# Optimization experiments

Hardware: AMD Instinct MI355X
Metric: run time of the kernel (lower is better)

The kernel has to match this reference:

```python
import jax, jax.numpy as jnp
import numpy as np

B, L, D = 8, 2048, 1024
PAD = 512  # trailing padded positions (zeros) to exercise the two padding masks


def setup_inputs() -> dict:
    key = jax.random.key(0)
    ks = jax.random.split(key, 11)
    q = jax.random.normal(ks[0], (B, L, D), dtype=jnp.float32)
    k = jax.random.normal(ks[1], (B, L, D), dtype=jnp.float32)
    v = jax.random.normal(ks[2], (B, L, D), dtype=jnp.float32)
    # zero-pad trailing positions (module infers masks from zero rows)
    q = q.at[:, L - PAD:, :].set(0.0)
    k = k.at[:, L - PAD:, :].set(0.0)
    v = v.at[:, L - PAD:, :].set(0.0)
    s = 1.0 / np.sqrt(D)
    Wq = jax.random.normal(ks[3], (D, D), dtype=jnp.float32) * s
    bq = jax.random.normal(ks[4], (D,), dtype=jnp.float32) * 0.01
    Wk = jax.random.normal(ks[5], (D, D), dtype=jnp.float32) * s
    bk = jax.random.normal(ks[6], (D,), dtype=jnp.float32) * 0.01
    Wv = jax.random.normal(ks[7], (D, D), dtype=jnp.float32) * s
    bv = jax.random.normal(ks[8], (D,), dtype=jnp.float32) * 0.01
    Wo = jax.random.normal(ks[9], (D, D), dtype=jnp.float32) * s
    bo = jax.random.normal(ks[10], (D,), dtype=jnp.float32) * 0.01
    return {"q": q, "k": k, "v": v, "Wq": Wq, "bq": bq, "Wk": Wk, "bk": bk,
            "Wv": Wv, "bv": bv, "Wo": Wo, "bo": bo}


def reference(q, k, v, Wq, bq, Wk, bk, Wv, bv, Wo, bo):
    # masks computed from raw (pre-projection) q, k, exactly like padding_mask_k/_q
    # bmm(ones_like(q), k^T)[b,i,j] == sum_d k[b,j,d]  -> mask where k row sums to 0
    attn_mask = (jnp.sum(k, axis=-1) == 0.0)[:, None, :]      # [B,1,Lk] -> broadcast [B,Lq,Lk]
    softmax_mask = (jnp.sum(q, axis=-1) == 0.0)[:, :, None]    # [B,Lq,1]

    qp = q @ Wq.T + bq  # torch Linear: x W^T + b
    kp = k @ Wk.T + bk
    vp = v @ Wv.T + bv

    scale = vp.shape[-1] ** -0.5  # original overwrites passed `scale`
    att = jnp.einsum('bqd,bkd->bqk', qp, kp) * scale           # [B,Lq,Lk]
    att = jnp.where(attn_mask, -jnp.inf, att)
    att = jax.nn.softmax(att, axis=-1)
    att = jnp.where(softmax_mask, 0.0, att)

    out = jnp.einsum('bqk,bkd->bqd', att, vp)                  # [B,Lq,D]
    out = out @ Wo.T + bo
    x = out + qp  # residual uses the PROJECTED q
    # LayerNorm, elementwise_affine=False, eps=1e-5
    mu = jnp.mean(x, axis=-1, keepdims=True)
    var = jnp.mean(jnp.square(x - mu), axis=-1, keepdims=True)
    return (x - mu) / jnp.sqrt(var + 1e-5)
```

## Files before the change

kernel.cpp:

```cpp
#include <hip/hip_runtime.h>
#include <stdint.h>

typedef unsigned short u16;
typedef __attribute__((ext_vector_type(8))) short short8;
typedef __attribute__((ext_vector_type(4))) float f32x4;

#define B_ 8
#define L_ 2048
#define D_ 1024

__device__ __forceinline__ u16 f2bf(float f) {
    unsigned int u = __float_as_uint(f);
    u = u + 0x7FFFu + ((u >> 16) & 1u);
    return (u16)(u >> 16);
}
__device__ __forceinline__ float bf2f(u16 h) {
    return __uint_as_float(((unsigned int)h) << 16);
}

struct CM3 {
    const float* s[3];
    u16* d[3];
    int* m[3];
};
__global__ __launch_bounds__(256) void convmask3_kernel(CM3 c) {
    int sel = blockIdx.y;
    const float* x = c.s[sel];
    u16* xb = c.d[sel];
    int* mask = c.m[sel];
    long row = blockIdx.x;
    int t = threadIdx.x;
    float4 v = ((const float4*)(x + row * D_))[t];
    ushort4 o;
    o.x = f2bf(v.x); o.y = f2bf(v.y); o.z = f2bf(v.z); o.w = f2bf(v.w);
    ((ushort4*)(xb + row * D_))[t] = o;
    float s = v.x + v.y + v.z + v.w;
    #pragma unroll
    for (int off = 32; off; off >>= 1) s += __shfl_down(s, off);
    __shared__ float sh[4];
    if ((t & 63) == 0) sh[t >> 6] = s;
    __syncthreads();
    if (t == 0) {
        float tot = sh[0] + sh[1] + sh[2] + sh[3];
        mask[row] = (tot == 0.0f) ? 1 : 0;
    }
}

struct Ptr4 { const float* s0; const float* s1; const float* s2; const float* s3; };
__global__ __launch_bounds__(256) void convert4_kernel(Ptr4 p, u16* __restrict__ dst) {
    const float* srcs[4] = {p.s0, p.s1, p.s2, p.s3};
    const float* src = srcs[blockIdx.y];
    u16* d = dst + (size_t)blockIdx.y * D_ * D_;
    int i = blockIdx.x * 256 + threadIdx.x;
    float4 v = ((const float4*)src)[i];
    ushort4 o;
    o.x = f2bf(v.x); o.y = f2bf(v.y); o.z = f2bf(v.z); o.w = f2bf(v.w);
    ((ushort4*)d)[i] = o;
}

__global__ __launch_bounds__(256) void flags_kernel(const int* __restrict__ mq,
                                                    const int* __restrict__ mk,
                                                    const int* __restrict__ mv,
                                                    int* __restrict__ q128,
                                                    int* __restrict__ k128,
                                                    int* __restrict__ v128,
                                                    int* __restrict__ k32) {
    int b = blockIdx.x, t = threadIdx.x;
    const int* src; int* dst; int g; int n;
    if (b < 128)      { src = mq; dst = q128; g = b;       n = 128; }
    else if (b < 256) { src = mk; dst = k128; g = b - 128; n = 128; }
    else if (b < 384) { src = mv; dst = v128; g = b - 256; n = 128; }
    else              { src = mk; dst = k32;  g = b - 384; n = 32;  }
    int val = (t < n) ? src[(long)g * n + t] : 1;
    __shared__ int sh;
    if (t == 0) sh = 1;
    __syncthreads();
    if (!val) sh = 0;
    __syncthreads();
    if (t == 0) dst[g] = sh;
}

__global__ __launch_bounds__(512) void packbits_kernel(const int* __restrict__ k32,
                                                       unsigned long long* __restrict__ kb) {
    int t = threadIdx.x;
    int b = t >> 6;
    int bit = t & 63;
    unsigned long long m = __ballot(k32[b * 64 + bit] == 0);
    if (bit == 0) kb[b] = m;
}

__device__ __forceinline__ void async_cp16(const void* g, void* l) {
    __builtin_amdgcn_global_load_lds((const __attribute__((address_space(1))) unsigned int*)g,
                                     (__attribute__((address_space(3))) unsigned int*)l,
                                     16, 0, 0);
}

struct P3 {
    const u16* A[3];
    u16* C[3];
    const float* bias[3];
    const int* rs[3];
};

#define GBM 128
#define GBN 128
#define GBK 32

#define STAGE(BUF, STEP)                                            \
    do {                                                            \
        const u16* pa_ = gA + (long)(STEP) * GBK;                   \
        const u16* pb_ = gB + (long)(STEP) * GBK;                   \
        async_cp16(pa_, &As[BUF][t * 8]);                           \
        async_cp16(pa_ + 64 * (long)K, &As[BUF][t * 8 + 2048]);     \
        async_cp16(pb_, &Bs[BUF][t * 8]);                           \
        async_cp16(pb_ + 64 * (long)K, &Bs[BUF][t * 8 + 2048]);     \
    } while (0)

template <int MODE>
__global__ __launch_bounds__(256, 3) void gemm_nt(const u16* __restrict__ A,
                                                  const u16* __restrict__ Bm,
                                                  void* __restrict__ C,
                                                  const float* __restrict__ bias,
                                                  const u16* __restrict__ resid,
                                                  const int* __restrict__ maskk,
                                                  int N, int K,
                                                  long strideA, long strideB, long strideC,
                                                  float scale,
                                                  const int* __restrict__ rowskip,
                                                  const int* __restrict__ colskip,
                                                  const unsigned long long* __restrict__ kbits,
                                                  int mblocks, int nblocks,
                                                  P3 p3) {
    __shared__ __align__(16) u16 As[2][GBM * GBK];
    __shared__ __align__(16) u16 Bs[2][GBN * GBK];

    int t = threadIdx.x;
    int lane = t & 63;
    int wave = t >> 6;
    int wr = wave >> 1;
    int wc = wave & 1;
    long m0 = (long)blockIdx.x * GBM;
    long n0 = (long)blockIdx.y * GBN;

    const u16* Ab;
    const u16* Bb;
    char* Cb;
    const float* biasp = bias;
    const int* rs;
    int rsidx;
    if (MODE == 0) {
        int z = blockIdx.z;
        Ab = p3.A[z];
        Bb = Bm + (long)z * D_ * D_;
        Cb = (char*)p3.C[z];
        biasp = p3.bias[z];
        rs = p3.rs[z];
        rsidx = blockIdx.x;
    } else {
        Ab = A + (long)blockIdx.z * strideA;
        Bb = Bm + (long)blockIdx.z * strideB;
        Cb = (char*)C + (long)blockIdx.z * strideC;
        rs = rowskip;
        rsidx = blockIdx.z * mblocks + blockIdx.x;
    }
    const int* mk = (MODE == 1) ? (maskk + (long)blockIdx.z * N) : nullptr;

    bool skipK = false;
    if (rs && rs[rsidx]) skipK = true;
    if (MODE == 1 && colskip && colskip[blockIdx.z * nblocks + blockIdx.y]) skipK = true;

    f32x4 acc[4][4] = {};

    int arow = t >> 2;
    int acol = ((t & 3) ^ ((t >> 3) & 3)) * 8;
    const u16* gA = Ab + (m0 + arow) * (long)K + acol;
    const u16* gB = Bb + (n0 + arow) * (long)K + acol;

    int mrow = wr * 64 + (lane & 15);
    int brow = wc * 64 + (lane & 15);
    int sw = ((lane >> 4) ^ ((lane >> 1) & 3)) * 8;

    if (!skipK) {
        unsigned long long bs = 0;
        int NT;
        if (MODE == 2) {
            bs = kbits[blockIdx.z];
            NT = __popcll(bs);
        } else {
            NT = K / GBK;
        }

        if (NT > 0) {
            int st;
            if (MODE == 2) { st = __builtin_ctzll(bs); bs &= bs - 1; } else st = 0;
            STAGE(0, st);

            for (int i = 0; i < NT; i++) {
                __syncthreads();
                if (i + 1 < NT) {
                    int stn;
                    if (MODE == 2) { stn = __builtin_ctzll(bs); bs &= bs - 1; } else stn = i + 1;
                    STAGE((i + 1) & 1, stn);
                }
                int b = i & 1;
                short8 af[4], bfr[4];
                #pragma unroll
                for (int ii = 0; ii < 4; ii++)
                    af[ii] = *(const short8*)&As[b][(mrow + ii * 16) * GBK + sw];
                #pragma unroll
                for (int jj = 0; jj < 4; jj++)
                    bfr[jj] = *(const short8*)&Bs[b][(brow + jj * 16) * GBK + sw];
                #pragma unroll
                for (int ii = 0; ii < 4; ii++)
                    #pragma unroll
                    for (int jj = 0; jj < 4; jj++)
                        acc[ii][jj] = __builtin_amdgcn_mfma_f32_16x16x32_bf16(
                            af[ii], bfr[jj], acc[ii][jj], 0, 0, 0);
            }
        }
    }

    #pragma unroll
    for (int ii = 0; ii < 4; ii++) {
        #pragma unroll
        for (int jj = 0; jj < 4; jj++) {
            long row = m0 + wr * 64 + ii * 16 + (lane >> 4) * 4;
            long col = n0 + wc * 64 + jj * 16 + (lane & 15);
            #pragma unroll
            for (int r = 0; r < 4; r++) {
                float vv = acc[ii][jj][r];
                long rr = row + r;
                if (MODE == 0) {
                    ((u16*)Cb)[rr * N + col] = f2bf(vv + biasp[col]);
                } else if (MODE == 1) {
                    float s = mk[col] ? -1e30f : vv * scale;
                    ((u16*)Cb)[rr * N + col] = f2bf(s);
                } else if (MODE == 2) {
                    ((u16*)Cb)[rr * N + col] = f2bf(vv);
                } else {
                    float x = vv + biasp[col] + bf2f(resid[rr * (long)N + col]);
                    ((u16*)Cb)[rr * N + col] = f2bf(x);
                }
            }
        }
    }
}

__global__ __launch_bounds__(256) void softmax_kernel(const u16* __restrict__ S,
                                                      u16* __restrict__ P,
                                                      const int* __restrict__ maskq) {
    long row = blockIdx.x;
    int t = threadIdx.x;
    const u16* Sr = S + row * L_;
    u16* Pr = P + row * L_;

    if (maskq[row]) {
        short8 z = {};
        *(short8*)&Pr[t * 8] = z;
        return;
    }

    short8 raw = *(const short8*)&Sr[t * 8];
    float s[8];
    #pragma unroll
    for (int e = 0; e < 8; e++) s[e] = bf2f((u16)raw[e]);

    float mx = s[0];
    #pragma unroll
    for (int e = 1; e < 8; e++) mx = fmaxf(mx, s[e]);
    #pragma unroll
    for (int off = 32; off; off >>= 1) mx = fmaxf(mx, __shfl_down(mx, off));
    __shared__ float sh[4];
    if ((t & 63) == 0) sh[t >> 6] = mx;
    __syncthreads();
    mx = fmaxf(fmaxf(sh[0], sh[1]), fmaxf(sh[2], sh[3]));
    __syncthreads();

    float e8[8], sum = 0.f;
    #pragma unroll
    for (int e = 0; e < 8; e++) { e8[e] = __expf(s[e] - mx); sum += e8[e]; }
    #pragma unroll
    for (int off = 32; off; off >>= 1) sum += __shfl_down(sum, off);
    if ((t & 63) == 0) sh[t >> 6] = sum;
    __syncthreads();
    sum = sh[0] + sh[1] + sh[2] + sh[3];
    float inv = 1.0f / sum;

    short8 o;
    #pragma unroll
    for (int e = 0; e < 8; e++) o[e] = (short)f2bf(e8[e] * inv);
    *(short8*)&Pr[t * 8] = o;
}

__global__ __launch_bounds__(256) void transpose_k(const u16* __restrict__ src,
                                                   u16* __restrict__ dst) {
    __shared__ u16 tile[32][34];
    long b = blockIdx.z;
    const u16* s = src + b * (long)L_ * D_;
    u16* d = dst + b * (long)L_ * D_;
    int gx = blockIdx.x * 32;
    int gy = blockIdx.y * 32;
    int tx = threadIdx.x, ty = threadIdx.y;
    #pragma unroll
    for (int r = 0; r < 32; r += 8)
        tile[ty + r][tx] = s[(long)(gy + ty + r) * D_ + gx + tx];
    __syncthreads();
    #pragma unroll
    for (int r = 0; r < 32; r += 8)
        d[(long)(gx + ty + r) * L_ + gy + tx] = tile[tx][ty + r];
}

__global__ __launch_bounds__(256) void layernorm_kernel(const u16* __restrict__ X,
                                                        float* __restrict__ O) {
    long row = blockIdx.x;
    int t = threadIdx.x;
    ushort4 u = ((const ushort4*)(X + row * D_))[t];
    float x0 = bf2f(u.x), x1 = bf2f(u.y), x2 = bf2f(u.z), x3 = bf2f(u.w);
    float s = x0 + x1 + x2 + x3;
    #pragma unroll
    for (int off = 32; off; off >>= 1) s += __shfl_down(s, off);
    __shared__ float sh[4];
    if ((t & 63) == 0) sh[t >> 6] = s;
    __syncthreads();
    float mu = (sh[0] + sh[1] + sh[2] + sh[3]) * (1.0f / D_);
    __syncthreads();

    float d0 = x0 - mu, d1 = x1 - mu, d2 = x2 - mu, d3 = x3 - mu;
    float ss = d0 * d0 + d1 * d1 + d2 * d2 + d3 * d3;
    #pragma unroll
    for (int off = 32; off; off >>= 1) ss += __shfl_down(ss, off);
    if ((t & 63) == 0) sh[t >> 6] = ss;
    __syncthreads();
    float var = (sh[0] + sh[1] + sh[2] + sh[3]) * (1.0f / D_);
    float rs = rsqrtf(var + 1e-5f);

    float4 o;
    o.x = d0 * rs; o.y = d1 * rs; o.z = d2 * rs; o.w = d3 * rs;
    ((float4*)(O + row * D_))[t] = o;
}

extern "C" void kernel_launch(void* const* d_in, const int* in_sizes, int n_in,
                              void* d_out, int out_size, void* d_ws, size_t ws_size,
                              hipStream_t stream) {
    const float* q  = (const float*)d_in[0];
    const float* k  = (const float*)d_in[1];
    const float* v  = (const float*)d_in[2];
    const float* Wq = (const float*)d_in[3];
    const float* bq = (const float*)d_in[4];
    const float* Wk = (const float*)d_in[5];
    const float* bk = (const float*)d_in[6];
    const float* Wv = (const float*)d_in[7];
    const float* bv = (const float*)d_in[8];
    const float* Wo = (const float*)d_in[9];
    const float* bo = (const float*)d_in[10];
    float* out = (float*)d_out;

    char* ws = (char*)d_ws;
    const size_t SZ = (size_t)B_ * L_ * D_ * 2;

    u16* qb   = (u16*)(ws + 0 * SZ);
    u16* kb   = (u16*)(ws + 1 * SZ);
    u16* vb   = (u16*)(ws + 2 * SZ);
    u16* vpb  = (u16*)(ws + 3 * SZ);
    u16* Sbuf = (u16*)(ws + 0 * SZ);
    u16* Pbuf = (u16*)(ws + 2 * SZ);
    u16* Obuf = (u16*)(ws + 0 * SZ);
    u16* Xbuf = (u16*)(ws + 2 * SZ);
    char* p = ws + 4 * SZ;
    u16* qpb = (u16*)p; p += SZ;
    u16* kpb = (u16*)p; p += SZ;
    u16* vpT = (u16*)p; p += SZ;
    u16* Wqb = (u16*)p; p += (size_t)D_ * D_ * 2;
    u16* Wkb = (u16*)p; p += (size_t)D_ * D_ * 2;
    u16* Wvb = (u16*)p; p += (size_t)D_ * D_ * 2;
    u16* Wob = (u16*)p; p += (size_t)D_ * D_ * 2;
    int* maskq = (int*)p; p += (size_t)B_ * L_ * 4;
    int* maskk = (int*)p; p += (size_t)B_ * L_ * 4;
    int* maskv = (int*)p; p += (size_t)B_ * L_ * 4;
    int* q128 = (int*)p; p += 128 * 4;
    int* k128 = (int*)p; p += 128 * 4;
    int* v128 = (int*)p; p += 128 * 4;
    int* kmask32 = (int*)p; p += 512 * 4;
    unsigned long long* kbits = (unsigned long long*)p; p += 8 * 8;

    P3 noP3 = {};

    CM3 cm;
    cm.s[0] = q;  cm.s[1] = k;  cm.s[2] = v;
    cm.d[0] = qb; cm.d[1] = kb; cm.d[2] = vb;
    cm.m[0] = maskq; cm.m[1] = maskk; cm.m[2] = maskv;
    convmask3_kernel<<<dim3(B_ * L_, 3), 256, 0, stream>>>(cm);
    Ptr4 wp{Wq, Wk, Wv, Wo};
    convert4_kernel<<<dim3(D_ * D_ / 4 / 256, 4), 256, 0, stream>>>(wp, Wqb);
    flags_kernel<<<896, 256, 0, stream>>>(maskq, maskk, maskv, q128, k128, v128, kmask32);
    packbits_kernel<<<1, 512, 0, stream>>>(kmask32, kbits);

    P3 pj;
    pj.A[0] = qb;  pj.A[1] = kb;  pj.A[2] = vb;
    pj.C[0] = qpb; pj.C[1] = kpb; pj.C[2] = vpb;
    pj.bias[0] = bq; pj.bias[1] = bk; pj.bias[2] = bv;
    pj.rs[0] = q128; pj.rs[1] = k128; pj.rs[2] = v128;
    gemm_nt<0><<<dim3(B_ * L_ / GBM, D_ / GBN, 3), 256, 0, stream>>>(
        nullptr, Wqb, nullptr, nullptr, nullptr, nullptr, D_, D_, 0, 0, 0, 0.f,
        nullptr, nullptr, nullptr, 0, 8, pj);

    transpose_k<<<dim3(D_ / 32, L_ / 32, B_), dim3(32, 8), 0, stream>>>(vpb, vpT);

    gemm_nt<1><<<dim3(L_ / GBM, L_ / GBN, B_), 256, 0, stream>>>(
        qpb, kpb, Sbuf, nullptr, nullptr, maskk, L_, D_,
        (long)L_ * D_, (long)L_ * D_, (long)L_ * L_ * 2, 0.03125f,
        q128, k128, nullptr, L_ / GBM, L_ / GBN, noP3);

    softmax_kernel<<<B_ * L_, 256, 0, stream>>>(Sbuf, Pbuf, maskq);

    gemm_nt<2><<<dim3(L_ / GBM, D_ / GBN, B_), 256, 0, stream>>>(
        Pbuf, vpT, Obuf, nullptr, nullptr, nullptr, D_, L_,
        (long)L_ * L_, (long)D_ * L_, (long)L_ * D_ * 2, 0.f,
        q128, nullptr, kbits, L_ / GBM, D_ / GBN, noP3);

    gemm_nt<3><<<dim3(B_ * L_ / GBM, D_ / GBN, 1), 256, 0, stream>>>(
        Obuf, Wob, Xbuf, bo, qpb, nullptr, D_, D_, 0, 0, 0, 0.f,
        q128, nullptr, nullptr, B_ * L_ / GBM, D_ / GBN, noP3);

    layernorm_kernel<<<B_ * L_, 256, 0, stream>>>(Xbuf, out);
}
```

Before: 593.9 us.

## Deepen GEMM pipeline to four LDS stages with register-prefetched fragments

The bf16 MFMA GEMM moves from a double-buffered LDS loop with a full __syncthreads per K-step to a four-slot ring. Three tiles are prefetched ahead, and explicit s_waitcnt vmcnt counts plus raw barriers replace the full synchronization. The A/B fragments for the next step are loaded into registers right after the current MFMAs, so LDS reads overlap compute. This aims to hide global-load latency, but it doubles LDS use per block and lowers the launch-bounds occupancy hint from 3 to 2 blocks. The hand-counted vmcnt values must exactly match the number of outstanding async loads per stage.

```diff
diff --git a/kernel.cpp b/kernel.cpp
--- a/kernel.cpp
+++ b/kernel.cpp
@@ -106,18 +106,18 @@
 #define GBN 128
 #define GBK 32
 
-#define STAGE(BUF, STEP)                                            \
-    do {                                                            \
-        const u16* pa_ = gA + (long)(STEP) * GBK;                   \
-        const u16* pb_ = gB + (long)(STEP) * GBK;                   \
-        async_cp16(pa_, &As[BUF][t * 8]);                           \
-        async_cp16(pa_ + 64 * (long)K, &As[BUF][t * 8 + 2048]);     \
-        async_cp16(pb_, &Bs[BUF][t * 8]);                           \
-        async_cp16(pb_ + 64 * (long)K, &Bs[BUF][t * 8 + 2048]);     \
+#define STAGE(SLOT, STEP)                                              \
+    do {                                                               \
+        const u16* pa_ = gA + (long)(STEP) * GBK;                      \
+        const u16* pb_ = gB + (long)(STEP) * GBK;                      \
+        async_cp16(pa_, &As[SLOT][t * 8]);                             \
+        async_cp16(pa_ + 64 * (long)K, &As[SLOT][t * 8 + 2048]);       \
+        async_cp16(pb_, &Bs[SLOT][t * 8]);                             \
+        async_cp16(pb_ + 64 * (long)K, &Bs[SLOT][t * 8 + 2048]);       \
     } while (0)
 
 template <int MODE>
-__global__ __launch_bounds__(256, 3) void gemm_nt(const u16* __restrict__ A,
+__global__ __launch_bounds__(256, 2) void gemm_nt(const u16* __restrict__ A,
                                                   const u16* __restrict__ Bm,
                                                   void* __restrict__ C,
                                                   const float* __restrict__ bias,
@@ -131,8 +131,8 @@
                                                   const unsigned long long* __restrict__ kbits,
                                                   int mblocks, int nblocks,
                                                   P3 p3) {
-    __shared__ __align__(16) u16 As[2][GBM * GBK];
-    __shared__ __align__(16) u16 Bs[2][GBN * GBK];
+    __shared__ __align__(16) u16 As[4][GBM * GBK];
+    __shared__ __align__(16) u16 Bs[4][GBN * GBK];
 
     int t = threadIdx.x;
     int lane = t & 63;
@@ -191,31 +191,52 @@
         }
 
         if (NT > 0) {
-            int st;
-            if (MODE == 2) { st = __builtin_ctzll(bs); bs &= bs - 1; } else st = 0;
-            STAGE(0, st);
+            int npro = NT < 3 ? NT : 3;
+            for (int s = 0; s < npro; s++) {
+                int st;
+                if (MODE == 2) { st = __builtin_ctzll(bs); bs &= bs - 1; } else st = s;
+                STAGE(s, st);
+            }
+            if (NT > 2) asm volatile("s_waitcnt vmcnt(4)" ::: "memory");
+            else        asm volatile("s_waitcnt vmcnt(0)" ::: "memory");
+            __builtin_amdgcn_s_barrier();
+            asm volatile("" ::: "memory");
+
+            short8 af[4], bfr[4];
+            #pragma unroll
+            for (int ii = 0; ii < 4; ii++)
+                af[ii] = *(const short8*)&As[0][(mrow + ii * 16) * GBK + sw];
+            #pragma unroll
+            for (int jj = 0; jj < 4; jj++)
+                bfr[jj] = *(const short8*)&Bs[0][(brow + jj * 16) * GBK + sw];
 
             for (int i = 0; i < NT; i++) {
-                __syncthreads();
-                if (i + 1 < NT) {
-                    int stn;
-                    if (MODE == 2) { stn = __builtin_ctzll(bs); bs &= bs - 1; } else stn = i + 1;
-                    STAGE((i + 1) & 1, stn);
+                if (i + 3 < NT) {
+                    int st;
+                    if (MODE == 2) { st = __builtin_ctzll(bs); bs &= bs - 1; } else st = i + 3;
+                    STAGE((i + 3) & 3, st);
                 }
-                int b = i & 1;
-                short8 af[4], bfr[4];
-                #pragma unroll
-                for (int ii = 0; ii < 4; ii++)
-                    af[ii] = *(const short8*)&As[b][(mrow + ii * 16) * GBK + sw];
-                #pragma unroll
-                for (int jj = 0; jj < 4; jj++)
-                    bfr[jj] = *(const short8*)&Bs[b][(brow + jj * 16) * GBK + sw];
                 #pragma unroll
                 for (int ii = 0; ii < 4; ii++)
                     #pragma unroll
                     for (int jj = 0; jj < 4; jj++)
                         acc[ii][jj] = __builtin_amdgcn_mfma_f32_16x16x32_bf16(
                             af[ii], bfr[jj], acc[ii][jj], 0, 0, 0);
+                if (i + 1 < NT) {
+                    int sl = (i + 1) & 3;
+                    #pragma unroll
+                    for (int ii = 0; ii < 4; ii++)
+                        af[ii] = *(const short8*)&As[sl][(mrow + ii * 16) * GBK + sw];
+                    #pragma unroll
+                    for (int jj = 0; jj < 4; jj++)
+                        bfr[jj] = *(const short8*)&Bs[sl][(brow + jj * 16) * GBK + sw];
+                }
+                if (i + 2 < NT) {
+                    if (i + 3 < NT) asm volatile("s_waitcnt vmcnt(4)" ::: "memory");
+                    else            asm volatile("s_waitcnt vmcnt(0)" ::: "memory");
+                    __builtin_amdgcn_s_barrier();
+                    asm volatile("" ::: "memory");
+                }
             }
         }
     }
```

Result: no change. 599.9 us (+1.0%).
